# Performance work log

Hardware: AMD Instinct MI355X
Metric: run time of the kernel (lower is better)

Reference implementation:

```python
import jax, jax.numpy as jnp
import numpy as np

N_NODES = 100000
N_EDGES = 3200000
N_GRAPHS = 64


def setup_inputs() -> dict:
    key = jax.random.key(0)
    ks = jax.random.split(key, 9)
    x = jax.random.normal(ks[0], (N_NODES, 3), dtype=jnp.float32)
    edge_index = jax.random.randint(ks[1], (2, N_EDGES), 0, N_NODES, dtype=jnp.int64)
    batch = jnp.sort(jax.random.randint(ks[2], (N_NODES,), 0, N_GRAPHS, dtype=jnp.int64))
    s1 = 1.0 / np.sqrt(3.0)
    s2 = 1.0 / np.sqrt(64.0)
    W1 = jax.random.normal(ks[3], (3, 64), dtype=jnp.float32) * s1
    b1 = jax.random.normal(ks[4], (64,), dtype=jnp.float32) * 0.02
    W2 = jax.random.normal(ks[5], (64, 64), dtype=jnp.float32) * s2
    b2 = jax.random.normal(ks[6], (64,), dtype=jnp.float32) * 0.02
    Wr = jax.random.normal(ks[7], (64, 1), dtype=jnp.float32) * s2
    br = jax.random.normal(ks[8], (1,), dtype=jnp.float32) * 0.02
    return {"x": x, "edge_index": edge_index, "batch": batch,
            "W1": W1, "b1": b1, "W2": W2, "b2": b2, "Wr": Wr, "br": br}


def reference(x, edge_index, batch, W1, b1, W2, b2, Wr, br):
    N = x.shape[0]
    # GCN normalization with self-loops: A_hat = D^-1/2 (A+I) D^-1/2
    loop = jnp.arange(N, dtype=edge_index.dtype)
    src = jnp.concatenate([edge_index[0], loop])  # message sources
    dst = jnp.concatenate([edge_index[1], loop])  # aggregation targets
    deg = jax.ops.segment_sum(jnp.ones(src.shape, jnp.float32), dst, num_segments=N)
    dinv = jnp.where(deg > 0, jax.lax.rsqrt(deg), 0.0)
    norm = dinv[src] * dinv[dst]  # [E+N]

    def conv(h):  # h: [N, F] -> gather, scale, scatter-add
        return jax.ops.segment_sum(norm[:, None] * h[src], dst, num_segments=N)

    h = jax.nn.relu(conv(x @ W1) + b1)
    # dropout(p=0.5) is identity in eval mode
    h = jax.nn.relu(conv(h @ W2) + b2)
    # global mean pool over graphs
    counts = jax.ops.segment_sum(jnp.ones((N,), jnp.float32), batch, num_segments=N_GRAPHS)
    pooled = jax.ops.segment_sum(h, batch, num_segments=N_GRAPHS) / jnp.maximum(counts, 1.0)[:, None]
    return pooled @ Wr + br
```

## Files before the change

### kernel.cpp

```cpp
#include <hip/hip_runtime.h>

#define N_NODES  100000
#define N_EDGES  3200000
#define N_GRAPHS 64
#define NBUCK 391
#define BSH   8
#define TILE  4096
#define CSR_CAP 9216

typedef float v2f __attribute__((ext_vector_type(2)));

__device__ __forceinline__ unsigned pk8(float a, float b, float c, float d) {
    int r = 0;
    r = __builtin_amdgcn_cvt_pk_fp8_f32(a, b, r, false);
    r = __builtin_amdgcn_cvt_pk_fp8_f32(c, d, r, true);
    return (unsigned)r;
}
__device__ __forceinline__ void addfp8(float4& a, unsigned u) {
    v2f lo = __builtin_amdgcn_cvt_pk_f32_fp8((int)u, false);
    v2f hi = __builtin_amdgcn_cvt_pk_f32_fp8((int)u, true);
    a.x += lo[0]; a.y += lo[1]; a.z += hi[0]; a.w += hi[1];
}
__device__ __forceinline__ void fma4(float4& c, float s, const float4& w) {
    c.x += s * w.x; c.y += s * w.y; c.z += s * w.z; c.w += s * w.w;
}

__global__ __launch_bounds__(1024) void k_split(
        const int* __restrict__ src, const int* __restrict__ dst,
        int* __restrict__ gcur, unsigned int* __restrict__ ebuf, int E) {
    __shared__ int hist[512];
    __shared__ int excl_s[512];
    __shared__ int base[NBUCK];
    __shared__ int curs[NBUCK];
    __shared__ int wtot[8];
    __shared__ unsigned int stg[TILE];
    __shared__ unsigned short bkt[TILE];
    int t = threadIdx.x;
    if (t < 512) hist[t] = 0;
    __syncthreads();

    int e0 = blockIdx.x * TILE;
    int nvalid = min(TILE, E - e0);
    int es[4], ed[4];
#pragma unroll
    for (int k = 0; k < 4; ++k) {
        int i = e0 + t + k * 1024;
        if (i < E) {
            es[k] = src[i]; ed[k] = dst[i];
            atomicAdd(&hist[ed[k] >> BSH], 1);
        } else { es[k] = 0; ed[k] = -1; }
    }
    __syncthreads();
    int v = (t < 512) ? hist[t] : 0;
    int lane = t & 63, wvi = t >> 6;
    int val = v;
    for (int off = 1; off < 64; off <<= 1) {
        int u = __shfl_up(val, off);
        if (lane >= off) val += u;
    }
    if (t < 512 && lane == 63) wtot[wvi] = val;
    __syncthreads();
    if (t < 512) {
        int woff = 0;
        for (int w = 0; w < wvi; ++w) woff += wtot[w];
        int texcl = woff + val - v;
        excl_s[t] = texcl;
        if (t < NBUCK) {
            if (v > 0) base[t] = atomicAdd(&gcur[t], v);
            curs[t] = 0;
        }
    }
    __syncthreads();
#pragma unroll
    for (int k = 0; k < 4; ++k) {
        if (ed[k] >= 0) {
            int b = ed[k] >> BSH;
            int r = atomicAdd(&curs[b], 1);
            int pos = excl_s[b] + r;
            stg[pos] = ((unsigned)(ed[k] & 255) << 24) | (unsigned)es[k];
            bkt[pos] = (unsigned short)b;
        }
    }
    __syncthreads();
    for (int j = t; j < nvalid; j += 1024) {
        unsigned p = stg[j];
        int b = bkt[j];
        int pos = base[b] + (j - excl_s[b]);
        if (pos < CSR_CAP) ebuf[(size_t)b * CSR_CAP + pos] = p;
    }
}

__global__ __launch_bounds__(1024) void k_csr(
        const unsigned int* __restrict__ ebuf, const int* __restrict__ gcur,
        int* __restrict__ rowptr, float* __restrict__ dinv, float4* __restrict__ y4,
        const float* __restrict__ x, int* __restrict__ csr_src, int N) {
    __shared__ int ncnt[256];
    __shared__ int nbase[256];
    __shared__ int ncur[256];
    __shared__ int wtot[4];
    __shared__ int sbase;
    __shared__ int stg[CSR_CAP];
    int b = blockIdx.x, t = threadIdx.x;
    int node0 = b << BSH;
    int nodes = min(256, N - node0);
    int cntE = min(gcur[b], CSR_CAP);
    const unsigned int* eb = ebuf + (size_t)b * CSR_CAP;
    if (t < 64) {
        int acc = 0;
        for (int i = t; i < b; i += 64) acc += min(gcur[i], CSR_CAP);
        for (int off = 32; off > 0; off >>= 1) acc += __shfl_down(acc, off);
        if (t == 0) sbase = acc;
    }
    if (t < 256) { ncnt[t] = 0; ncur[t] = 0; }
    __syncthreads();
    int base = sbase;
    if (b == NBUCK - 1 && t == 0) rowptr[N_NODES] = base + cntE;
    for (int j = t; j < cntE; j += 1024) atomicAdd(&ncnt[(int)(eb[j] >> 24)], 1);
    __syncthreads();
    int v = (t < 256) ? ncnt[t] : 0;
    if (t < 256) {
        int lane = t & 63, wv = t >> 6;
        int val = v;
        for (int off = 1; off < 64; off <<= 1) {
            int u = __shfl_up(val, off);
            if (lane >= off) val += u;
        }
        if (lane == 63) wtot[wv] = val;
        __syncthreads();
        int woff = 0;
        for (int w = 0; w < wv; ++w) woff += wtot[w];
        int excl = woff + val - v;
        nbase[t] = excl;
        if (t < nodes) {
            int nn = node0 + t;
            rowptr[nn] = base + excl;
            float dn = rsqrtf((float)(v + 1));
            dinv[nn] = dn;
            y4[nn] = make_float4(dn * x[nn * 3 + 0], dn * x[nn * 3 + 1], dn * x[nn * 3 + 2], 0.f);
        }
    } else {
        __syncthreads();
    }
    __syncthreads();
    for (int j = t; j < cntE; j += 1024) {
        unsigned p = eb[j];
        int ln = (int)(p >> 24);
        int r = atomicAdd(&ncur[ln], 1);
        stg[nbase[ln] + r] = (int)(p & 0xFFFFFFu);
    }
    __syncthreads();
    for (int j = t; j < cntE; j += 1024) csr_src[(size_t)base + j] = stg[j];
}

__global__ __launch_bounds__(256) void k_agg3h1(
        const float4* __restrict__ y4, const int* __restrict__ csr_src,
        const int* __restrict__ rowptr, const float* __restrict__ dinv,
        const float* __restrict__ W1, const float* __restrict__ b1,
        uint4* __restrict__ Hs, int N) {
    int tid = blockIdx.x * blockDim.x + threadIdx.x;
    int n = tid >> 2, q = tid & 3;
    if (n >= N) return;
    int beg = rowptr[n], end = rowptr[n + 1];
    float ax0 = 0.f, ay0 = 0.f, az0 = 0.f;
    float ax1 = 0.f, ay1 = 0.f, az1 = 0.f;
    float ax2 = 0.f, ay2 = 0.f, az2 = 0.f;
    float ax3 = 0.f, ay3 = 0.f, az3 = 0.f;
    if (end > beg) {
        for (int c = beg; c < end; c += 32) {
            int idx[8];
#pragma unroll
            for (int j = 0; j < 8; ++j)
                idx[j] = csr_src[min(c + 4 * j + q, end - 1)];
            float4 v[8];
#pragma unroll
            for (int j = 0; j < 8; ++j) v[j] = y4[idx[j]];
#pragma unroll
            for (int j = 0; j < 8; ++j) {
                bool ok = (c + 4 * j + q) < end;
                float vx = ok ? v[j].x : 0.f;
                float vy = ok ? v[j].y : 0.f;
                float vz = ok ? v[j].z : 0.f;
                if ((j & 3) == 0) { ax0 += vx; ay0 += vy; az0 += vz; }
                if ((j & 3) == 1) { ax1 += vx; ay1 += vy; az1 += vz; }
                if ((j & 3) == 2) { ax2 += vx; ay2 += vy; az2 += vz; }
                if ((j & 3) == 3) { ax3 += vx; ay3 += vy; az3 += vz; }
            }
        }
    }
    float rx = (ax0 + ax1) + (ax2 + ax3);
    float ry = (ay0 + ay1) + (ay2 + ay3);
    float rz = (az0 + az1) + (az2 + az3);
    for (int off = 1; off < 4; off <<= 1) {
        rx += __shfl_xor(rx, off);
        ry += __shfl_xor(ry, off);
        rz += __shfl_xor(rz, off);
    }
    float dn = dinv[n];
    float4 self = y4[n];
    float A0 = dn * (rx + self.x), A1 = dn * (ry + self.y), A2 = dn * (rz + self.z);
    unsigned vals[4];
#pragma unroll
    for (int g = 0; g < 4; ++g) {
        int f = 16 * q + 4 * g;
        float w0 = dn * fmaxf(A0 * W1[f]     + A1 * W1[64 + f]     + A2 * W1[128 + f]     + b1[f],     0.f);
        float w1 = dn * fmaxf(A0 * W1[f + 1] + A1 * W1[64 + f + 1] + A2 * W1[128 + f + 1] + b1[f + 1], 0.f);
        float w2 = dn * fmaxf(A0 * W1[f + 2] + A1 * W1[64 + f + 2] + A2 * W1[128 + f + 2] + b1[f + 2], 0.f);
        float w3 = dn * fmaxf(A0 * W1[f + 3] + A1 * W1[64 + f + 3] + A2 * W1[128 + f + 3] + b1[f + 3], 0.f);
        vals[g] = pk8(w0, w1, w2, w3);
    }
    Hs[(size_t)n * 4 + q] = make_uint4(vals[0], vals[1], vals[2], vals[3]);
}

__global__ __launch_bounds__(512) void k_aggmm(
        const unsigned int* __restrict__ Hs, const int* __restrict__ csr_src,
        const int* __restrict__ rowptr, const float* __restrict__ dinv,
        const float4* __restrict__ W2v, const float* __restrict__ b2,
        const float* __restrict__ Wr, const int* __restrict__ batch,
        float* __restrict__ gsum, float* __restrict__ gcnt, int N) {
    __shared__ float4 W2s[1024];
    __shared__ float lsum[N_GRAPHS];
    __shared__ float lcnt[N_GRAPHS];
    int t = threadIdx.x;
    for (int i = t; i < 1024; i += 512) W2s[i] = W2v[i];
    if (t < N_GRAPHS) { lsum[t] = 0.f; lcnt[t] = 0.f; }
    __syncthreads();

    int tid = blockIdx.x * 512 + t;
    int n = tid >> 4, q = tid & 15;
    int lane = t & 63;
    int base = lane & ~15;
    int beg = rowptr[n], end = rowptr[n + 1];
    float4 acc0 = make_float4(0.f, 0.f, 0.f, 0.f);
    float4 acc1 = make_float4(0.f, 0.f, 0.f, 0.f);
    float4 acc2 = make_float4(0.f, 0.f, 0.f, 0.f);
    float4 acc3 = make_float4(0.f, 0.f, 0.f, 0.f);
    if (end > beg) {
        int myidx = csr_src[min(beg + q, end - 1)];
        for (int c = beg; c < end; c += 16) {
            int nxt = csr_src[min(c + 16 + q, end - 1)];
            unsigned u[16];
#pragma unroll
            for (int j = 0; j < 16; ++j) {
                int s = __shfl(myidx, base + j);
                u[j] = Hs[(size_t)s * 16 + q];
            }
            int m = end - c;
#pragma unroll
            for (int j = 0; j < 16; ++j) {
                unsigned uj = (j < m) ? u[j] : 0u;
                if ((j & 3) == 0) addfp8(acc0, uj);
                if ((j & 3) == 1) addfp8(acc1, uj);
                if ((j & 3) == 2) addfp8(acc2, uj);
                if ((j & 3) == 3) addfp8(acc3, uj);
            }
            myidx = nxt;
        }
    }
    addfp8(acc0, Hs[(size_t)n * 16 + q]);
    float dn = dinv[n];
    float4 r;
    r.x = dn * ((acc0.x + acc1.x) + (acc2.x + acc3.x));
    r.y = dn * ((acc0.y + acc1.y) + (acc2.y + acc3.y));
    r.z = dn * ((acc0.z + acc1.z) + (acc2.z + acc3.z));
    r.w = dn * ((acc0.w + acc1.w) + (acc2.w + acc3.w));

    float4 bb = ((const float4*)b2)[q];
    float4 wr = ((const float4*)Wr)[q];
    float4 cacc = make_float4(0.f, 0.f, 0.f, 0.f);
#pragma unroll 4
    for (int ks = 0; ks < 16; ++ks) {
        float ax = __shfl(r.x, base + ks);
        float ay = __shfl(r.y, base + ks);
        float az = __shfl(r.z, base + ks);
        float aw = __shfl(r.w, base + ks);
        fma4(cacc, ax, W2s[(4 * ks + 0) * 16 + q]);
        fma4(cacc, ay, W2s[(4 * ks + 1) * 16 + q]);
        fma4(cacc, az, W2s[(4 * ks + 2) * 16 + q]);
        fma4(cacc, aw, W2s[(4 * ks + 3) * 16 + q]);
    }
    float p = fmaxf(cacc.x + bb.x, 0.f) * wr.x + fmaxf(cacc.y + bb.y, 0.f) * wr.y +
              fmaxf(cacc.z + bb.z, 0.f) * wr.z + fmaxf(cacc.w + bb.w, 0.f) * wr.w;
    p += __shfl_xor(p, 1);
    p += __shfl_xor(p, 2);
    p += __shfl_xor(p, 4);
    p += __shfl_xor(p, 8);
    if (q == 0) {
        int g = batch[n];
        atomicAdd(&lsum[g], p);
        atomicAdd(&lcnt[g], 1.f);
    }
    __syncthreads();
    if (t < N_GRAPHS && lcnt[t] > 0.0f) {
        atomicAdd(&gsum[t], lsum[t]);
        atomicAdd(&gcnt[t], lcnt[t]);
    }
}

__global__ void k_out(const float* __restrict__ gsum, const float* __restrict__ gcnt,
                      const float* __restrict__ br, float* __restrict__ out) {
    int g = threadIdx.x;
    if (g < N_GRAPHS) out[g] = gsum[g] / fmaxf(gcnt[g], 1.0f) + br[0];
}

extern "C" void kernel_launch(void* const* d_in, const int* in_sizes, int n_in,
                              void* d_out, int out_size, void* d_ws, size_t ws_size,
                              hipStream_t stream) {
    const float* x     = (const float*)d_in[0];
    const int*   ei    = (const int*)d_in[1];
    const int*   batch = (const int*)d_in[2];
    const float* W1    = (const float*)d_in[3];
    const float* b1    = (const float*)d_in[4];
    const float* W2    = (const float*)d_in[5];
    const float* b2    = (const float*)d_in[6];
    const float* Wr    = (const float*)d_in[7];
    const float* br    = (const float*)d_in[8];
    float* out = (float*)d_out;

    const int N = N_NODES, E = N_EDGES;
    const int* src = ei;
    const int* dst = ei + E;

    char* w = (char*)d_ws;
    float* A        = (float*)w; w += (size_t)N * 64 * sizeof(float);
    unsigned int* Hs = (unsigned int*)w; w += (size_t)N * 64;
    int*   csr_src  = (int*)w;   w += (size_t)E * sizeof(int);
    float* dinv     = (float*)w; w += (size_t)N * sizeof(float);
    int*   rowptr   = (int*)w;   w += (size_t)(N + 1) * sizeof(int);
    int*   gcur     = (int*)w;   w += (size_t)NBUCK * sizeof(int);
    float* gsum     = (float*)w; w += N_GRAPHS * sizeof(float);
    float* gcnt     = (float*)w; w += N_GRAPHS * sizeof(float);
    float4* y4      = (float4*)w; w += (size_t)N * sizeof(float4);
    unsigned int* ebuf = (unsigned int*)A;

    hipMemsetAsync(gcur, 0, (size_t)NBUCK * sizeof(int), stream);
    hipMemsetAsync(gsum, 0, N_GRAPHS * sizeof(float), stream);
    hipMemsetAsync(gcnt, 0, N_GRAPHS * sizeof(float), stream);

    k_split<<<(E + TILE - 1) / TILE, 1024, 0, stream>>>(src, dst, gcur, ebuf, E);
    k_csr<<<NBUCK, 1024, 0, stream>>>(ebuf, gcur, rowptr, dinv, y4, x, csr_src, N);

    k_agg3h1<<<(N * 4 + 255) / 256, 256, 0, stream>>>(y4, csr_src, rowptr, dinv,
                                                      W1, b1, (uint4*)Hs, N);

    k_aggmm<<<(N * 16) / 512, 512, 0, stream>>>(Hs, csr_src, rowptr, dinv,
                                                (const float4*)W2, b2, Wr, batch,
                                                gsum, gcnt, N);

    k_out<<<1, 64, 0, stream>>>(gsum, gcnt, br, out);
}
```

Before: 214.3 us.

## Fuse layer-1 aggregation into CSR build using global degree atomics

Degrees are now counted with global atomics in the split kernel, and a new small kernel computes dinv and the scaled input features before CSR construction. The layer-1 gather, W1 transform and fp8 packing are then done inside the CSR kernel, reading neighbor indices straight from shared memory instead of re-reading csr_src from global memory in a separate kernel. This saves one kernel launch and a pass over the edge list. In exchange it adds 3.2M global atomics on random destinations plus an extra memset and launch, and the layer-1 work is limited to 391 blocks with only 4 lanes per node.

```diff
diff --git a/kernel.cpp b/kernel.cpp
--- a/kernel.cpp
+++ b/kernel.cpp
@@ -27,7 +27,8 @@
 
 __global__ __launch_bounds__(1024) void k_split(
         const int* __restrict__ src, const int* __restrict__ dst,
-        int* __restrict__ gcur, unsigned int* __restrict__ ebuf, int E) {
+        int* __restrict__ gcur, unsigned int* __restrict__ ebuf,
+        unsigned int* __restrict__ deg, int E) {
     __shared__ int hist[512];
     __shared__ int excl_s[512];
     __shared__ int base[NBUCK];
@@ -48,6 +49,7 @@
         if (i < E) {
             es[k] = src[i]; ed[k] = dst[i];
             atomicAdd(&hist[ed[k] >> BSH], 1);
+            atomicAdd(&deg[ed[k]], 1u);
         } else { es[k] = 0; ed[k] = -1; }
     }
     __syncthreads();
@@ -90,10 +92,22 @@
     }
 }
 
-__global__ __launch_bounds__(1024) void k_csr(
+__global__ void k_prep(const unsigned int* __restrict__ deg, const float* __restrict__ x,
+                       float* __restrict__ dinv, float4* __restrict__ y4, int N) {
+    int n = blockIdx.x * 256 + threadIdx.x;
+    if (n < N) {
+        float dn = rsqrtf((float)deg[n] + 1.0f);
+        dinv[n] = dn;
+        y4[n] = make_float4(dn * x[3 * n], dn * x[3 * n + 1], dn * x[3 * n + 2], 0.f);
+    }
+}
+
+__global__ __launch_bounds__(1024, 8) void k_csr(
         const unsigned int* __restrict__ ebuf, const int* __restrict__ gcur,
-        int* __restrict__ rowptr, float* __restrict__ dinv, float4* __restrict__ y4,
-        const float* __restrict__ x, int* __restrict__ csr_src, int N) {
+        int* __restrict__ rowptr, const float* __restrict__ dinv,
+        const float4* __restrict__ y4, int* __restrict__ csr_src,
+        const float* __restrict__ W1, const float* __restrict__ b1,
+        uint4* __restrict__ Hs, int N) {
     __shared__ int ncnt[256];
     __shared__ int nbase[256];
     __shared__ int ncur[256];
@@ -131,13 +145,7 @@
         for (int w = 0; w < wv; ++w) woff += wtot[w];
         int excl = woff + val - v;
         nbase[t] = excl;
-        if (t < nodes) {
-            int nn = node0 + t;
-            rowptr[nn] = base + excl;
-            float dn = rsqrtf((float)(v + 1));
-            dinv[nn] = dn;
-            y4[nn] = make_float4(dn * x[nn * 3 + 0], dn * x[nn * 3 + 1], dn * x[nn * 3 + 2], 0.f);
-        }
+        if (t < nodes) rowptr[node0 + t] = base + excl;
     } else {
         __syncthreads();
     }
@@ -150,65 +158,57 @@
     }
     __syncthreads();
     for (int j = t; j < cntE; j += 1024) csr_src[(size_t)base + j] = stg[j];
-}
-
-__global__ __launch_bounds__(256) void k_agg3h1(
-        const float4* __restrict__ y4, const int* __restrict__ csr_src,
-        const int* __restrict__ rowptr, const float* __restrict__ dinv,
-        const float* __restrict__ W1, const float* __restrict__ b1,
-        uint4* __restrict__ Hs, int N) {
-    int tid = blockIdx.x * blockDim.x + threadIdx.x;
-    int n = tid >> 2, q = tid & 3;
-    if (n >= N) return;
-    int beg = rowptr[n], end = rowptr[n + 1];
-    float ax0 = 0.f, ay0 = 0.f, az0 = 0.f;
-    float ax1 = 0.f, ay1 = 0.f, az1 = 0.f;
-    float ax2 = 0.f, ay2 = 0.f, az2 = 0.f;
-    float ax3 = 0.f, ay3 = 0.f, az3 = 0.f;
-    if (end > beg) {
-        for (int c = beg; c < end; c += 32) {
-            int idx[8];
-#pragma unroll
-            for (int j = 0; j < 8; ++j)
-                idx[j] = csr_src[min(c + 4 * j + q, end - 1)];
-            float4 v[8];
-#pragma unroll
-            for (int j = 0; j < 8; ++j) v[j] = y4[idx[j]];
-#pragma unroll
-            for (int j = 0; j < 8; ++j) {
-                bool ok = (c + 4 * j + q) < end;
-                float vx = ok ? v[j].x : 0.f;
-                float vy = ok ? v[j].y : 0.f;
-                float vz = ok ? v[j].z : 0.f;
-                if ((j & 3) == 0) { ax0 += vx; ay0 += vy; az0 += vz; }
-                if ((j & 3) == 1) { ax1 += vx; ay1 += vy; az1 += vz; }
-                if ((j & 3) == 2) { ax2 += vx; ay2 += vy; az2 += vz; }
-                if ((j & 3) == 3) { ax3 += vx; ay3 += vy; az3 += vz; }
-            }
-        }
-    }
-    float rx = (ax0 + ax1) + (ax2 + ax3);
-    float ry = (ay0 + ay1) + (ay2 + ay3);
-    float rz = (az0 + az1) + (az2 + az3);
-    for (int off = 1; off < 4; off <<= 1) {
-        rx += __shfl_xor(rx, off);
-        ry += __shfl_xor(ry, off);
-        rz += __shfl_xor(rz, off);
-    }
-    float dn = dinv[n];
-    float4 self = y4[n];
-    float A0 = dn * (rx + self.x), A1 = dn * (ry + self.y), A2 = dn * (rz + self.z);
-    unsigned vals[4];
-#pragma unroll
-    for (int g = 0; g < 4; ++g) {
-        int f = 16 * q + 4 * g;
-        float w0 = dn * fmaxf(A0 * W1[f]     + A1 * W1[64 + f]     + A2 * W1[128 + f]     + b1[f],     0.f);
-        float w1 = dn * fmaxf(A0 * W1[f + 1] + A1 * W1[64 + f + 1] + A2 * W1[128 + f + 1] + b1[f + 1], 0.f);
-        float w2 = dn * fmaxf(A0 * W1[f + 2] + A1 * W1[64 + f + 2] + A2 * W1[128 + f + 2] + b1[f + 2], 0.f);
-        float w3 = dn * fmaxf(A0 * W1[f + 3] + A1 * W1[64 + f + 3] + A2 * W1[128 + f + 3] + b1[f + 3], 0.f);
-        vals[g] = pk8(w0, w1, w2, w3);
-    }
-    Hs[(size_t)n * 4 + q] = make_uint4(vals[0], vals[1], vals[2], vals[3]);
+
+    {
+        int i = t >> 2, q = t & 3;
+        if (i < nodes) {
+            int nn = node0 + i;
+            int beg = nbase[i];
+            int cnt = ncnt[i];
+            float sx0 = 0.f, sy0 = 0.f, sz0 = 0.f;
+            float sx1 = 0.f, sy1 = 0.f, sz1 = 0.f;
+            if (cnt > 0) {
+                for (int c = 0; c < cnt; c += 16) {
+                    int idx[4];
+#pragma unroll
+                    for (int k = 0; k < 4; ++k)
+                        idx[k] = stg[beg + min(c + 4 * k + q, cnt - 1)];
+                    float4 vv[4];
+#pragma unroll
+                    for (int k = 0; k < 4; ++k) vv[k] = y4[idx[k]];
+#pragma unroll
+                    for (int k = 0; k < 4; ++k) {
+                        bool ok = (c + 4 * k + q) < cnt;
+                        float fx = ok ? vv[k].x : 0.f;
+                        float fy = ok ? vv[k].y : 0.f;
+                        float fz = ok ? vv[k].z : 0.f;
+                        if (k & 1) { sx1 += fx; sy1 += fy; sz1 += fz; }
+                        else       { sx0 += fx; sy0 += fy; sz0 += fz; }
+                    }
+                }
+            }
+            float rx = sx0 + sx1, ry = sy0 + sy1, rz = sz0 + sz1;
+            for (int off = 1; off < 4; off <<= 1) {
+                rx += __shfl_xor(rx, off);
+                ry += __shfl_xor(ry, off);
+                rz += __shfl_xor(rz, off);
+            }
+            float dn = dinv[nn];
+            float4 self = y4[nn];
+            float A0 = dn * (rx + self.x), A1 = dn * (ry + self.y), A2 = dn * (rz + self.z);
+            unsigned vals[4];
+#pragma unroll
+            for (int g = 0; g < 4; ++g) {
+                int f = 16 * q + 4 * g;
+                float w0 = dn * fmaxf(A0 * W1[f]     + A1 * W1[64 + f]     + A2 * W1[128 + f]     + b1[f],     0.f);
+                float w1 = dn * fmaxf(A0 * W1[f + 1] + A1 * W1[64 + f + 1] + A2 * W1[128 + f + 1] + b1[f + 1], 0.f);
+                float w2 = dn * fmaxf(A0 * W1[f + 2] + A1 * W1[64 + f + 2] + A2 * W1[128 + f + 2] + b1[f + 2], 0.f);
+                float w3 = dn * fmaxf(A0 * W1[f + 3] + A1 * W1[64 + f + 3] + A2 * W1[128 + f + 3] + b1[f + 3], 0.f);
+                vals[g] = pk8(w0, w1, w2, w3);
+            }
+            Hs[(size_t)nn * 4 + q] = make_uint4(vals[0], vals[1], vals[2], vals[3]);
+        }
+    }
 }
 
 __global__ __launch_bounds__(512) void k_aggmm(
@@ -330,17 +330,18 @@
     float* gsum     = (float*)w; w += N_GRAPHS * sizeof(float);
     float* gcnt     = (float*)w; w += N_GRAPHS * sizeof(float);
     float4* y4      = (float4*)w; w += (size_t)N * sizeof(float4);
+    unsigned int* deg = (unsigned int*)w; w += (size_t)N * sizeof(unsigned int);
     unsigned int* ebuf = (unsigned int*)A;
 
     hipMemsetAsync(gcur, 0, (size_t)NBUCK * sizeof(int), stream);
+    hipMemsetAsync(deg, 0, (size_t)N * sizeof(unsigned int), stream);
     hipMemsetAsync(gsum, 0, N_GRAPHS * sizeof(float), stream);
     hipMemsetAsync(gcnt, 0, N_GRAPHS * sizeof(float), stream);
 
-    k_split<<<(E + TILE - 1) / TILE, 1024, 0, stream>>>(src, dst, gcur, ebuf, E);
-    k_csr<<<NBUCK, 1024, 0, stream>>>(ebuf, gcur, rowptr, dinv, y4, x, csr_src, N);
-
-    k_agg3h1<<<(N * 4 + 255) / 256, 256, 0, stream>>>(y4, csr_src, rowptr, dinv,
-                                                      W1, b1, (uint4*)Hs, N);
+    k_split<<<(E + TILE - 1) / TILE, 1024, 0, stream>>>(src, dst, gcur, ebuf, deg, E);
+    k_prep<<<(N + 255) / 256, 256, 0, stream>>>(deg, x, dinv, y4, N);
+    k_csr<<<NBUCK, 1024, 0, stream>>>(ebuf, gcur, rowptr, dinv, y4, csr_src,
+                                      W1, b1, (uint4*)Hs, N);
 
     k_aggmm<<<(N * 16) / 512, 512, 0, stream>>>(Hs, csr_src, rowptr, dinv,
                                                 (const float4*)W2, b2, Wr, batch,
```

Result: slower. 333.1 us (+55.4%).
